# Optimization experiments

Measured on AMD Instinct MI355X. Metric: run time of the kernel, lower is better.

Reference implementation:

```python
import jax, jax.numpy as jnp
import numpy as np

TWO_PI = 2.0 * np.pi
DT = 0.01            # self.dt buffer
COE_D, COE_M = 2, 8  # interp_degree, interp_mesh_size (per dim) for coe fitters
NL_D, NL_M = 4, 40   # nonlinear fitter degree / mesh_size
NL_A, NL_B = -15.0, 15.0  # nonlinear_interp_mesh_bound


def lagrange_basis(t, d):
    """Degree-d Lagrange basis at local coord t in [0,1]; returns [..., d+1]."""
    nodes = jnp.arange(d + 1, dtype=t.dtype) / d
    basis = []
    for j in range(d + 1):
        L = jnp.ones_like(t)
        for k in range(d + 1):
            if k != j:
                L = L * (t - nodes[k]) / (nodes[j] - nodes[k])
        basis.append(L)
    return jnp.stack(basis, axis=-1)


def interp_cells(x, a, b, m, d):
    """Map x to (cell index [..,], basis values [.., d+1]) on an m-cell mesh over [a,b]."""
    s = (x - a) / (b - a) * m
    cell = jnp.clip(jnp.floor(s), 0, m - 1)
    t = s - cell  # allows extrapolation outside [a,b] via edge cells
    return cell.astype(jnp.int32), lagrange_basis(t, d)


def nonlinear_interp(w, x):
    """1D piecewise-Lagrange fitter applied elementwise (nonlinearfitter)."""
    cell, L = interp_cells(x, NL_A, NL_B, NL_M, NL_D)
    idx = cell[..., None] * NL_D + jnp.arange(NL_D + 1)
    return jnp.sum(w[idx] * L, axis=-1)


def coe_fields(ws, xy):
    """2D tensor-product Lagrange interp on fixed inputs xy -> [C,H,W] coef fields."""
    c0, L0 = interp_cells(xy[..., 0], 0.0, TWO_PI, COE_M, COE_D)
    c1, L1 = interp_cells(xy[..., 1], 0.0, TWO_PI, COE_M, COE_D)
    i0 = c0[..., None] * COE_D + jnp.arange(COE_D + 1)   # [H,W,d+1]
    i1 = c1[..., None] * COE_D + jnp.arange(COE_D + 1)
    wloc = ws[:, i0[..., :, None], i1[..., None, :]]     # [C,H,W,d+1,d+1]
    return jnp.einsum('chwij,hwi,hwj->chw', wloc, L0, L1)


def conv_same(u, k):
    """u: [B,H,W], k: [N,1,kh,kw] -> [B,N,H,W] with zero (Dirichlet) padding."""
    return jax.lax.conv_general_dilated(u[:, None], k, (1, 1), 'SAME',
                                        dimension_numbers=('NCHW', 'OIHW', 'NCHW'))


def setup_inputs() -> dict:
    key = jax.random.key(0)
    ks = jax.random.split(key, 5)
    B, H, W, K, N = 16, 512, 512, 5, 6
    init = jax.random.normal(ks[0], (B, H, W), jnp.float32)
    delta = jnp.zeros((1, 1, K, K), jnp.float32).at[0, 0, K // 2, K // 2].set(1.0)
    idkernel = delta + 0.01 * jax.random.normal(ks[1], (1, 1, K, K), jnp.float32)
    fdkernel = 0.1 * jax.random.normal(ks[2], (N, 1, K, K), jnp.float32)
    M = COE_M * COE_D + 1
    coe_w = 0.1 * jax.random.normal(ks[3], (N - 1, M, M), jnp.float32)
    nl_w = 0.1 * jax.random.normal(ks[4], (NL_M * NL_D + 1,), jnp.float32)
    gx = jnp.linspace(0.0, TWO_PI, H, endpoint=False).astype(jnp.float32)
    xy = jnp.stack(jnp.meshgrid(gx, gx, indexing='ij'), axis=-1)  # [H,W,2]
    return {"init": init, "idkernel": idkernel, "fdkernel": fdkernel,
            "coe_w": coe_w, "nl_w": nl_w, "xy": xy, "stepnum": 8}


def reference(init, idkernel, fdkernel, coe_w, nl_w, xy, stepnum):
    # coefficient fields are evaluated once (fixed xy), as in the torch forward
    coe = coe_fields(coe_w, xy)[None]  # [1, N-1, H, W], broadcasts over batch

    def step(u, _):
        uid = conv_same(u, idkernel)[:, 0]           # [B,H,W]
        ufd = conv_same(u, fdkernel)                 # [B,N,H,W]
        un = uid + DT * ((coe * ufd[:, 1:]).sum(axis=1)
                         + nonlinear_interp(nl_w, ufd[:, 0]))
        return un, None

    u, _ = jax.lax.scan(step, init, None, length=stepnum)
    return u
```

## Files before the change

### kernel.cpp

```cpp
#include <hip/hip_runtime.h>

typedef float f2 __attribute__((ext_vector_type(2)));

static constexpr int HH = 512;
static constexpr int WW = 512;
static constexpr int HW = HH * WW;
static constexpr int NB = 16;
static constexpr float DT_F = 0.01f;
static constexpr float TWO_PI_F = 6.283185307179586f;

static constexpr int TW = 32;
static constexpr int TH = 16;
static constexpr int SWx = TW + 4;
static constexpr int SHx = TH + 4;
static constexpr int NTASK = SHx * 10 * 2;

__device__ const float NLM[5][5] = {
    {1.0f,      -25.0f/3.0f,   70.0f/3.0f,  -80.0f/3.0f,   32.0f/3.0f},
    {0.0f,       16.0f,      -208.0f/3.0f,   96.0f,      -128.0f/3.0f},
    {0.0f,      -12.0f,        76.0f,      -128.0f,        64.0f},
    {0.0f,   16.0f/3.0f,    -112.0f/3.0f,  224.0f/3.0f, -128.0f/3.0f},
    {0.0f,      -1.0f,       22.0f/3.0f,   -16.0f,        32.0f/3.0f},
};

__device__ __forceinline__ void pkfma_s(f2& acc, f2 w, f2 u) {
    asm("v_pk_fma_f32 %0, %1, %2, %0" : "+v"(acc) : "s"(w), "v"(u));
}
__device__ __forceinline__ void pkfma_v(f2& acc, f2 a, f2 b) {
    asm("v_pk_fma_f32 %0, %1, %2, %0" : "+v"(acc) : "v"(a), "v"(b));
}

__device__ __forceinline__ float nl_eval(const float* __restrict__ snlp, float x)
{
    const float sc = fmaf(x, 4.0f / 3.0f, 20.0f);
    const float cf = fminf(fmaxf(floorf(sc), 0.0f), 39.0f);
    const float t = sc - cf;
    const int base = (int)cf * 8;
    const float4 cm = *reinterpret_cast<const float4*>(&snlp[base]);
    const float cm4 = snlp[base + 4];
    float r = fmaf(cm4, t, cm.w);
    r = fmaf(r, t, cm.z);
    r = fmaf(r, t, cm.y);
    r = fmaf(r, t, cm.x);
    return r;
}

__global__ __launch_bounds__(256) void keff_kernel(const float* __restrict__ coe_w,
                                                   const float* __restrict__ xy,
                                                   const float* __restrict__ fdk,
                                                   float* __restrict__ keff)
{
    __shared__ float sw[5 * 17 * 17];
    for (int i = threadIdx.x; i < 5 * 17 * 17; i += 256) sw[i] = coe_w[i];
    __syncthreads();

    int p = blockIdx.x * 256 + threadIdx.x;
    if (p >= HW) return;

    float x0 = xy[2 * p + 0];
    float x1 = xy[2 * p + 1];

    float s0 = x0 / TWO_PI_F * 8.0f;
    float c0f = fminf(fmaxf(floorf(s0), 0.0f), 7.0f);
    float t0 = s0 - c0f;
    int i0 = 2 * (int)c0f;

    float s1 = x1 / TWO_PI_F * 8.0f;
    float c1f = fminf(fmaxf(floorf(s1), 0.0f), 7.0f);
    float t1 = s1 - c1f;
    int i1 = 2 * (int)c1f;

    float L0[3], L1[3];
    L0[0] = (t0 - 0.5f) * (t0 - 1.0f) * 2.0f;
    L0[1] = t0 * (t0 - 1.0f) * -4.0f;
    L0[2] = t0 * (t0 - 0.5f) * 2.0f;
    L1[0] = (t1 - 0.5f) * (t1 - 1.0f) * 2.0f;
    L1[1] = t1 * (t1 - 1.0f) * -4.0f;
    L1[2] = t1 * (t1 - 0.5f) * 2.0f;

    float coe[5];
    #pragma unroll
    for (int c = 0; c < 5; ++c) {
        float acc = 0.0f;
        #pragma unroll
        for (int i = 0; i < 3; ++i) {
            #pragma unroll
            for (int j = 0; j < 3; ++j) {
                acc = fmaf(sw[c * 289 + (i0 + i) * 17 + (i1 + j)], L0[i] * L1[j], acc);
            }
        }
        coe[c] = acc;
    }

    #pragma unroll
    for (int t = 0; t < 25; ++t) {
        float v = coe[0] * fdk[25 + t];
        v = fmaf(coe[1], fdk[50 + t], v);
        v = fmaf(coe[2], fdk[75 + t], v);
        v = fmaf(coe[3], fdk[100 + t], v);
        v = fmaf(coe[4], fdk[125 + t], v);
        keff[t * HW + p] = v;
    }
}

__device__ __forceinline__ float4 ld_u(const float* __restrict__ u,
                                       int row0, int col0, int idx)
{
    const int lr = idx / 10;
    const int j  = idx - 10 * lr;
    const int gr = row0 - 2 + lr;
    const int gc = col0 - 4 + 4 * j;
    float4 v = make_float4(0.f, 0.f, 0.f, 0.f);
    if (gr >= 0 && gr < HH && gc >= 0 && gc + 3 < WW)
        v = *reinterpret_cast<const float4*>(u + gr * WW + gc);
    return v;
}
__device__ __forceinline__ void st_u(float* __restrict__ su2, int idx, float4 v)
{
    const int lr = idx / 10;
    const int j  = idx - 10 * lr;
    float* row = su2 + lr * SWx;
    if (j == 0) {
        *reinterpret_cast<float2*>(row) = make_float2(v.z, v.w);
    } else if (j == 9) {
        *reinterpret_cast<float2*>(row + 34) = make_float2(v.x, v.y);
    } else {
        *reinterpret_cast<float2*>(row + 4 * j - 2) = make_float2(v.x, v.y);
        *reinterpret_cast<float2*>(row + 4 * j)     = make_float2(v.z, v.w);
    }
}

__global__ __launch_bounds__(256) void step_kernel(
    const float* __restrict__ uin,
    float* __restrict__ uout,
    const float* __restrict__ kid,
    const float* __restrict__ kfd,
    const float* __restrict__ nlw,
    const float* __restrict__ keff)
{
    __shared__ float su[2][2][SHx * SWx];
    __shared__ float snlp[40 * 8];

    const int tid = threadIdx.x;
    const int bx = blockIdx.x & 15;
    const int by = blockIdx.x >> 4;
    const int col0 = bx * TW;
    const int row0 = by * TH;

    const int bh  = tid >> 7;
    const int q   = tid & 127;
    const int t8  = q & 7;
    const int tyr = q >> 3;
    const int c4  = 4 * t8;
    const int p0  = (row0 + tyr) * WW + col0 + c4;

    if (tid < 200) {
        const int c = tid / 5;
        const int m = tid - 5 * c;
        float a = nlw[4 * c + 0] * NLM[0][m];
        a = fmaf(nlw[4 * c + 1], NLM[1][m], a);
        a = fmaf(nlw[4 * c + 2], NLM[2][m], a);
        a = fmaf(nlw[4 * c + 3], NLM[3][m], a);
        a = fmaf(nlw[4 * c + 4], NLM[4][m], a);
        snlp[c * 8 + m] = a;
    }

    f2 ke[25][2];
    #pragma unroll
    for (int t = 0; t < 25; ++t) {
        const float4 kv = *reinterpret_cast<const float4*>(keff + t * HW + p0);
        ke[t][0] = (f2){kv.x, kv.y};
        ke[t][1] = (f2){kv.z, kv.w};
    }

    const int task0 = tid;
    const int task1 = tid + 256;
    const bool has1 = task1 < NTASK;
    const int t0h = task0 >= 200;
    const int i0x = task0 - 200 * t0h;
    const int t1h = 1;
    const int i1x = task1 - 200;

    float4 s0 = ld_u(uin + (size_t)(t0h * 8 + 0) * HW, row0, col0, i0x);
    float4 s1 = has1 ? ld_u(uin + (size_t)(t1h * 8 + 0) * HW, row0, col0, i1x)
                     : make_float4(0.f, 0.f, 0.f, 0.f);
    st_u(su[0][t0h], i0x, s0);
    if (has1) st_u(su[0][t1h], i1x, s1);

    for (int b = 0; b < 8; ++b) {
        const int buf = b & 1;
        if (b < 7) {
            s0 = ld_u(uin + (size_t)(t0h * 8 + b + 1) * HW, row0, col0, i0x);
            if (has1) s1 = ld_u(uin + (size_t)(t1h * 8 + b + 1) * HW, row0, col0, i1x);
        }
        __syncthreads();

        const float* base = su[buf][bh] + tyr * SWx + c4;
        f2 aid[2], af0[2], aef[2];
        aid[0] = (f2){0.f, 0.f}; aid[1] = (f2){0.f, 0.f};
        af0[0] = (f2){0.f, 0.f}; af0[1] = (f2){0.f, 0.f};
        aef[0] = (f2){0.f, 0.f}; aef[1] = (f2){0.f, 0.f};

        #pragma unroll
        for (int dy = 0; dy < 5; ++dy) {
            const float4 w0 = *reinterpret_cast<const float4*>(base + dy * SWx);
            const float4 w1 = *reinterpret_cast<const float4*>(base + dy * SWx + 4);
            const f2 r01 = (f2){w0.x, w0.y};
            const f2 r23 = (f2){w0.z, w0.w};
            const f2 r45 = (f2){w1.x, w1.y};
            const f2 r67 = (f2){w1.z, w1.w};
            const f2 r12 = (f2){w0.y, w0.z};
            const f2 r34 = (f2){w0.w, w1.x};
            const f2 r56 = (f2){w1.y, w1.z};

            #define CONV_DX(DX, PL, PH)                                      \
            {                                                                 \
                const int o = dy * 5 + (DX);                                  \
                f2 wv;                                                        \
                wv.x = kid[o]; wv.y = wv.x;                                   \
                pkfma_s(aid[0], wv, PL); pkfma_s(aid[1], wv, PH);             \
                wv.x = kfd[o]; wv.y = wv.x;                                   \
                pkfma_s(af0[0], wv, PL); pkfma_s(af0[1], wv, PH);             \
                pkfma_v(aef[0], ke[o][0], PL);                                \
                pkfma_v(aef[1], ke[o][1], PH);                                \
            }
            CONV_DX(0, r01, r23)
            CONV_DX(1, r12, r34)
            CONV_DX(2, r23, r45)
            CONV_DX(3, r34, r56)
            CONV_DX(4, r45, r67)
            #undef CONV_DX
        }

        const float xs[4]  = {af0[0].x, af0[0].y, af0[1].x, af0[1].y};
        const float efv[4] = {aef[0].x, aef[0].y, aef[1].x, aef[1].y};
        const float idv[4] = {aid[0].x, aid[0].y, aid[1].x, aid[1].y};
        float outv[4];
        #pragma unroll
        for (int k = 0; k < 4; ++k) {
            const float nl = nl_eval(snlp, xs[k]);
            outv[k] = fmaf(DT_F, efv[k] + nl, idv[k]);
        }
        *reinterpret_cast<float4*>(uout + (size_t)(b + 8 * bh) * HW + p0) =
            make_float4(outv[0], outv[1], outv[2], outv[3]);

        if (b < 7) {
            st_u(su[buf ^ 1][t0h], i0x, s0);
            if (has1) st_u(su[buf ^ 1][t1h], i1x, s1);
        }
    }
}

extern "C" void kernel_launch(void* const* d_in, const int* in_sizes, int n_in,
                              void* d_out, int out_size, void* d_ws, size_t ws_size,
                              hipStream_t stream)
{
    const float* init = (const float*)d_in[0];
    const float* idk  = (const float*)d_in[1];
    const float* fdk  = (const float*)d_in[2];
    const float* coew = (const float*)d_in[3];
    const float* nlw  = (const float*)d_in[4];
    const float* xy   = (const float*)d_in[5];

    float* keff = (float*)d_ws;
    float* uA   = keff + 25 * HW;
    float* outp = (float*)d_out;

    keff_kernel<<<(HW + 255) / 256, 256, 0, stream>>>(coew, xy, fdk, keff);

    const int nblk = (WW / TW) * (HH / TH);
    const float* src = init;
    for (int s = 0; s < 8; ++s) {
        float* dst = (s & 1) ? outp : uA;
        step_kernel<<<nblk, 256, 0, stream>>>(src, dst, idk, fdk, nlw, keff);
        src = dst;
    }
}
```

Baseline: 186.2 us.

## Halve tile width to 16 columns with two outputs per thread

Shrinks the block tile from 32x16 to 16x16, so each thread computes two adjacent outputs instead of four. This halves the per-thread effective-kernel register array and the accumulators, which should allow more waves per CU and better latency hiding. The halo staging is simplified to aligned float4 copies into a 24-wide shared tile, replacing the split float2 stores. In exchange the halo fraction rises, twice as many blocks are needed, and global keff loads and output stores become narrower 8-byte accesses.

```diff
diff --git a/kernel.cpp b/kernel.cpp
--- a/kernel.cpp
+++ b/kernel.cpp
@@ -5,15 +5,14 @@
 static constexpr int HH = 512;
 static constexpr int WW = 512;
 static constexpr int HW = HH * WW;
-static constexpr int NB = 16;
 static constexpr float DT_F = 0.01f;
 static constexpr float TWO_PI_F = 6.283185307179586f;
 
-static constexpr int TW = 32;
+static constexpr int TW = 16;
 static constexpr int TH = 16;
-static constexpr int SWx = TW + 4;
-static constexpr int SHx = TH + 4;
-static constexpr int NTASK = SHx * 10 * 2;
+static constexpr int SWx = 24;
+static constexpr int SHx = 20;
+static constexpr int NST = SHx * 6;
 
 __device__ const float NLM[5][5] = {
     {1.0f,      -25.0f/3.0f,   70.0f/3.0f,  -80.0f/3.0f,   32.0f/3.0f},
@@ -103,33 +102,6 @@
     }
 }
 
-__device__ __forceinline__ float4 ld_u(const float* __restrict__ u,
-                                       int row0, int col0, int idx)
-{
-    const int lr = idx / 10;
-    const int j  = idx - 10 * lr;
-    const int gr = row0 - 2 + lr;
-    const int gc = col0 - 4 + 4 * j;
-    float4 v = make_float4(0.f, 0.f, 0.f, 0.f);
-    if (gr >= 0 && gr < HH && gc >= 0 && gc + 3 < WW)
-        v = *reinterpret_cast<const float4*>(u + gr * WW + gc);
-    return v;
-}
-__device__ __forceinline__ void st_u(float* __restrict__ su2, int idx, float4 v)
-{
-    const int lr = idx / 10;
-    const int j  = idx - 10 * lr;
-    float* row = su2 + lr * SWx;
-    if (j == 0) {
-        *reinterpret_cast<float2*>(row) = make_float2(v.z, v.w);
-    } else if (j == 9) {
-        *reinterpret_cast<float2*>(row + 34) = make_float2(v.x, v.y);
-    } else {
-        *reinterpret_cast<float2*>(row + 4 * j - 2) = make_float2(v.x, v.y);
-        *reinterpret_cast<float2*>(row + 4 * j)     = make_float2(v.z, v.w);
-    }
-}
-
 __global__ __launch_bounds__(256) void step_kernel(
     const float* __restrict__ uin,
     float* __restrict__ uout,
@@ -142,8 +114,8 @@
     __shared__ float snlp[40 * 8];
 
     const int tid = threadIdx.x;
-    const int bx = blockIdx.x & 15;
-    const int by = blockIdx.x >> 4;
+    const int bx = blockIdx.x & 31;
+    const int by = blockIdx.x >> 5;
     const int col0 = bx * TW;
     const int row0 = by * TH;
 
@@ -151,8 +123,8 @@
     const int q   = tid & 127;
     const int t8  = q & 7;
     const int tyr = q >> 3;
-    const int c4  = 4 * t8;
-    const int p0  = (row0 + tyr) * WW + col0 + c4;
+    const int c2  = 2 * t8;
+    const int p0  = (row0 + tyr) * WW + col0 + c2;
 
     if (tid < 200) {
         const int c = tid / 5;
@@ -165,89 +137,77 @@
         snlp[c * 8 + m] = a;
     }
 
-    f2 ke[25][2];
+    f2 ke[25];
     #pragma unroll
-    for (int t = 0; t < 25; ++t) {
-        const float4 kv = *reinterpret_cast<const float4*>(keff + t * HW + p0);
-        ke[t][0] = (f2){kv.x, kv.y};
-        ke[t][1] = (f2){kv.z, kv.w};
-    }
-
-    const int task0 = tid;
-    const int task1 = tid + 256;
-    const bool has1 = task1 < NTASK;
-    const int t0h = task0 >= 200;
-    const int i0x = task0 - 200 * t0h;
-    const int t1h = 1;
-    const int i1x = task1 - 200;
-
-    float4 s0 = ld_u(uin + (size_t)(t0h * 8 + 0) * HW, row0, col0, i0x);
-    float4 s1 = has1 ? ld_u(uin + (size_t)(t1h * 8 + 0) * HW, row0, col0, i1x)
-                     : make_float4(0.f, 0.f, 0.f, 0.f);
-    st_u(su[0][t0h], i0x, s0);
-    if (has1) st_u(su[0][t1h], i1x, s1);
+    for (int t = 0; t < 25; ++t)
+        ke[t] = *reinterpret_cast<const f2*>(keff + t * HW + p0);
+
+    const bool hast = tid < 2 * NST;
+    const int th  = (tid >= NST) ? 1 : 0;
+    const int ix  = tid - NST * th;
+    const int lr  = ix / 6;
+    const int jb  = ix - 6 * lr;
+    const int gr  = row0 - 2 + lr;
+    const int gc  = col0 - 4 + 4 * jb;
+    const bool inb = (gr >= 0) & (gr < HH) & (gc >= 0) & (gc + 3 < WW);
+    const int goff = gr * WW + gc;
+    const int soff = lr * SWx + 4 * jb;
+
+    float4 s = make_float4(0.f, 0.f, 0.f, 0.f);
+    if (hast) {
+        if (inb) s = *reinterpret_cast<const float4*>(uin + (size_t)(th * 8) * HW + goff);
+        *reinterpret_cast<float4*>(su[0][th] + soff) = s;
+    }
 
     for (int b = 0; b < 8; ++b) {
         const int buf = b & 1;
-        if (b < 7) {
-            s0 = ld_u(uin + (size_t)(t0h * 8 + b + 1) * HW, row0, col0, i0x);
-            if (has1) s1 = ld_u(uin + (size_t)(t1h * 8 + b + 1) * HW, row0, col0, i1x);
+        if (b < 7 && hast) {
+            s = make_float4(0.f, 0.f, 0.f, 0.f);
+            if (inb) s = *reinterpret_cast<const float4*>(
+                uin + (size_t)(th * 8 + b + 1) * HW + goff);
         }
         __syncthreads();
 
-        const float* base = su[buf][bh] + tyr * SWx + c4;
-        f2 aid[2], af0[2], aef[2];
-        aid[0] = (f2){0.f, 0.f}; aid[1] = (f2){0.f, 0.f};
-        af0[0] = (f2){0.f, 0.f}; af0[1] = (f2){0.f, 0.f};
-        aef[0] = (f2){0.f, 0.f}; aef[1] = (f2){0.f, 0.f};
+        const float* base = su[buf][bh] + tyr * SWx + c2 + 2;
+        f2 aid = (f2){0.f, 0.f};
+        f2 af0 = (f2){0.f, 0.f};
+        f2 aef = (f2){0.f, 0.f};
 
         #pragma unroll
         for (int dy = 0; dy < 5; ++dy) {
-            const float4 w0 = *reinterpret_cast<const float4*>(base + dy * SWx);
-            const float4 w1 = *reinterpret_cast<const float4*>(base + dy * SWx + 4);
-            const f2 r01 = (f2){w0.x, w0.y};
-            const f2 r23 = (f2){w0.z, w0.w};
-            const f2 r45 = (f2){w1.x, w1.y};
-            const f2 r67 = (f2){w1.z, w1.w};
-            const f2 r12 = (f2){w0.y, w0.z};
-            const f2 r34 = (f2){w0.w, w1.x};
-            const f2 r56 = (f2){w1.y, w1.z};
-
-            #define CONV_DX(DX, PL, PH)                                      \
+            const f2 P0 = *reinterpret_cast<const f2*>(base + dy * SWx);
+            const f2 P2 = *reinterpret_cast<const f2*>(base + dy * SWx + 2);
+            const f2 P4 = *reinterpret_cast<const f2*>(base + dy * SWx + 4);
+            const f2 P1 = (f2){P0.y, P2.x};
+            const f2 P3 = (f2){P2.y, P4.x};
+
+            #define CONV_DX(DX, PP)                                          \
             {                                                                 \
                 const int o = dy * 5 + (DX);                                  \
                 f2 wv;                                                        \
                 wv.x = kid[o]; wv.y = wv.x;                                   \
-                pkfma_s(aid[0], wv, PL); pkfma_s(aid[1], wv, PH);             \
+                pkfma_s(aid, wv, PP);                                         \
                 wv.x = kfd[o]; wv.y = wv.x;                                   \
-                pkfma_s(af0[0], wv, PL); pkfma_s(af0[1], wv, PH);             \
-                pkfma_v(aef[0], ke[o][0], PL);                                \
-                pkfma_v(aef[1], ke[o][1], PH);                                \
+                pkfma_s(af0, wv, PP);                                         \
+                pkfma_v(aef, ke[o], PP);                                      \
             }
-            CONV_DX(0, r01, r23)
-            CONV_DX(1, r12, r34)
-            CONV_DX(2, r23, r45)
-            CONV_DX(3, r34, r56)
-            CONV_DX(4, r45, r67)
+            CONV_DX(0, P0)
+            CONV_DX(1, P1)
+            CONV_DX(2, P2)
+            CONV_DX(3, P3)
+            CONV_DX(4, P4)
             #undef CONV_DX
         }
 
-        const float xs[4]  = {af0[0].x, af0[0].y, af0[1].x, af0[1].y};
-        const float efv[4] = {aef[0].x, aef[0].y, aef[1].x, aef[1].y};
-        const float idv[4] = {aid[0].x, aid[0].y, aid[1].x, aid[1].y};
-        float outv[4];
-        #pragma unroll
-        for (int k = 0; k < 4; ++k) {
-            const float nl = nl_eval(snlp, xs[k]);
-            outv[k] = fmaf(DT_F, efv[k] + nl, idv[k]);
-        }
-        *reinterpret_cast<float4*>(uout + (size_t)(b + 8 * bh) * HW + p0) =
-            make_float4(outv[0], outv[1], outv[2], outv[3]);
-
-        if (b < 7) {
-            st_u(su[buf ^ 1][t0h], i0x, s0);
-            if (has1) st_u(su[buf ^ 1][t1h], i1x, s1);
-        }
+        const float nl0 = nl_eval(snlp, af0.x);
+        const float nl1 = nl_eval(snlp, af0.y);
+        f2 outv;
+        outv.x = fmaf(DT_F, aef.x + nl0, aid.x);
+        outv.y = fmaf(DT_F, aef.y + nl1, aid.y);
+        *reinterpret_cast<f2*>(uout + (size_t)(b + 8 * bh) * HW + p0) = outv;
+
+        if (b < 7 && hast)
+            *reinterpret_cast<float4*>(su[buf ^ 1][th] + soff) = s;
     }
 }
 
```

Measured after the change: 210.9 us. +13.3%, slower.

## Split batch loop across two block groups and pad shared strides

Applied to the files above, without the earlier changes.

Each step kernel now launches twice as many blocks, and each block handles 4 of the 8 batch slices per half instead of all 8. This raises parallelism and occupancy across CUs, at the cost of reloading the 25 per-pixel coefficient registers in twice as many blocks. The shared tile row stride is padded from 36 to 40 floats and the nonlinear coefficient table stride changes from 8 to 9 with scalar loads, presumably to reduce LDS bank conflicts.

```diff
diff --git a/kernel.cpp b/kernel.cpp
--- a/kernel.cpp
+++ b/kernel.cpp
@@ -5,15 +5,15 @@
 static constexpr int HH = 512;
 static constexpr int WW = 512;
 static constexpr int HW = HH * WW;
-static constexpr int NB = 16;
 static constexpr float DT_F = 0.01f;
 static constexpr float TWO_PI_F = 6.283185307179586f;
 
 static constexpr int TW = 32;
 static constexpr int TH = 16;
-static constexpr int SWx = TW + 4;
-static constexpr int SHx = TH + 4;
-static constexpr int NTASK = SHx * 10 * 2;
+static constexpr int SWx = 40;
+static constexpr int SHx = 20;
+static constexpr int NST = SHx * 10;
+static constexpr int NTASK = NST * 2;
 
 __device__ const float NLM[5][5] = {
     {1.0f,      -25.0f/3.0f,   70.0f/3.0f,  -80.0f/3.0f,   32.0f/3.0f},
@@ -35,13 +35,16 @@
     const float sc = fmaf(x, 4.0f / 3.0f, 20.0f);
     const float cf = fminf(fmaxf(floorf(sc), 0.0f), 39.0f);
     const float t = sc - cf;
-    const int base = (int)cf * 8;
-    const float4 cm = *reinterpret_cast<const float4*>(&snlp[base]);
-    const float cm4 = snlp[base + 4];
-    float r = fmaf(cm4, t, cm.w);
-    r = fmaf(r, t, cm.z);
-    r = fmaf(r, t, cm.y);
-    r = fmaf(r, t, cm.x);
+    const int base = (int)cf * 9;
+    const float c0 = snlp[base + 0];
+    const float c1 = snlp[base + 1];
+    const float c2 = snlp[base + 2];
+    const float c3 = snlp[base + 3];
+    const float c4 = snlp[base + 4];
+    float r = fmaf(c4, t, c3);
+    r = fmaf(r, t, c2);
+    r = fmaf(r, t, c1);
+    r = fmaf(r, t, c0);
     return r;
 }
 
@@ -139,11 +142,14 @@
     const float* __restrict__ keff)
 {
     __shared__ float su[2][2][SHx * SWx];
-    __shared__ float snlp[40 * 8];
+    __shared__ float snlp[40 * 9];
 
     const int tid = threadIdx.x;
-    const int bx = blockIdx.x & 15;
-    const int by = blockIdx.x >> 4;
+    const int bid = blockIdx.x;
+    const int g   = bid >> 9;
+    const int tix = bid & 511;
+    const int bx = tix & 15;
+    const int by = tix >> 4;
     const int col0 = bx * TW;
     const int row0 = by * TH;
 
@@ -162,7 +168,7 @@
         a = fmaf(nlw[4 * c + 2], NLM[2][m], a);
         a = fmaf(nlw[4 * c + 3], NLM[3][m], a);
         a = fmaf(nlw[4 * c + 4], NLM[4][m], a);
-        snlp[c * 8 + m] = a;
+        snlp[c * 9 + m] = a;
     }
 
     f2 ke[25][2];
@@ -176,22 +182,23 @@
     const int task0 = tid;
     const int task1 = tid + 256;
     const bool has1 = task1 < NTASK;
-    const int t0h = task0 >= 200;
-    const int i0x = task0 - 200 * t0h;
-    const int t1h = 1;
-    const int i1x = task1 - 200;
-
-    float4 s0 = ld_u(uin + (size_t)(t0h * 8 + 0) * HW, row0, col0, i0x);
-    float4 s1 = has1 ? ld_u(uin + (size_t)(t1h * 8 + 0) * HW, row0, col0, i1x)
+    const int t0h = task0 >= NST;
+    const int i0x = task0 - NST * t0h;
+    const int i1x = task1 - NST;
+
+    const int bbase = g * 4;
+
+    float4 s0 = ld_u(uin + (size_t)(t0h * 8 + bbase) * HW, row0, col0, i0x);
+    float4 s1 = has1 ? ld_u(uin + (size_t)(8 + bbase) * HW, row0, col0, i1x)
                      : make_float4(0.f, 0.f, 0.f, 0.f);
     st_u(su[0][t0h], i0x, s0);
-    if (has1) st_u(su[0][t1h], i1x, s1);
-
-    for (int b = 0; b < 8; ++b) {
+    if (has1) st_u(su[0][1], i1x, s1);
+
+    for (int b = 0; b < 4; ++b) {
         const int buf = b & 1;
-        if (b < 7) {
-            s0 = ld_u(uin + (size_t)(t0h * 8 + b + 1) * HW, row0, col0, i0x);
-            if (has1) s1 = ld_u(uin + (size_t)(t1h * 8 + b + 1) * HW, row0, col0, i1x);
+        if (b < 3) {
+            s0 = ld_u(uin + (size_t)(t0h * 8 + bbase + b + 1) * HW, row0, col0, i0x);
+            if (has1) s1 = ld_u(uin + (size_t)(8 + bbase + b + 1) * HW, row0, col0, i1x);
         }
         __syncthreads();
 
@@ -241,12 +248,12 @@
             const float nl = nl_eval(snlp, xs[k]);
             outv[k] = fmaf(DT_F, efv[k] + nl, idv[k]);
         }
-        *reinterpret_cast<float4*>(uout + (size_t)(b + 8 * bh) * HW + p0) =
+        *reinterpret_cast<float4*>(uout + (size_t)(bh * 8 + bbase + b) * HW + p0) =
             make_float4(outv[0], outv[1], outv[2], outv[3]);
 
-        if (b < 7) {
+        if (b < 3) {
             st_u(su[buf ^ 1][t0h], i0x, s0);
-            if (has1) st_u(su[buf ^ 1][t1h], i1x, s1);
+            if (has1) st_u(su[buf ^ 1][1], i1x, s1);
         }
     }
 }
@@ -268,7 +275,7 @@
 
     keff_kernel<<<(HW + 255) / 256, 256, 0, stream>>>(coew, xy, fdk, keff);
 
-    const int nblk = (WW / TW) * (HH / TH);
+    const int nblk = 1024;
     const float* src = init;
     for (int s = 0; s < 8; ++s) {
         float* dst = (s & 1) ? outp : uA;
```

After: 207.7 us (median of 5 runs). 1.12x slower.
